# Performance work log

Hardware: AMD Instinct MI355X
Metric: run time of the kernel (lower is better)

## Reference

```python
import jax, jax.numpy as jnp
import numpy as np

B, N, DIM = 2, 2048, 1024
HEADS = 16
DIM_HEAD = DIM // HEADS  # 64
SCALE = DIM_HEAD ** -0.5


def setup_inputs() -> dict:
    key = jax.random.key(0)
    k1, k2, k3 = jax.random.split(key, 3)
    x = jax.random.normal(k1, (B, N, DIM), dtype=jnp.float32)
    W_qkv = jax.random.normal(k2, (DIM, 3 * HEADS * DIM_HEAD), dtype=jnp.float32) * (DIM ** -0.5)
    W_out = jax.random.normal(k3, (HEADS * DIM_HEAD, DIM), dtype=jnp.float32) * (DIM ** -0.5)
    return {"x": x, "W_qkv": W_qkv, "W_out": W_out}


def reference(x, W_qkv, W_out):
    b, n, _ = x.shape
    qkv = jnp.einsum('bnd,de->bne', x, W_qkv)  # [b, n, 3*h*dh]
    # faithful to einops 'b n (d k h) -> k b h n d': last axis factored as (dh, 3, h)
    qkv = qkv.reshape(b, n, DIM_HEAD, 3, HEADS)
    qkv = jnp.transpose(qkv, (3, 0, 4, 1, 2))  # [3, b, h, n, dh]
    q, k, v = qkv[0], qkv[1], qkv[2]
    scores = jnp.einsum('bhid,bhjd->bhij', q, k) * SCALE  # [b, h, n, n]
    causal_mask = jnp.triu(jnp.ones((n, n), dtype=bool), k=1)
    scores = jnp.where(causal_mask, -jnp.inf, scores)
    attn = jax.nn.softmax(scores, axis=-1)
    out = jnp.einsum('bhij,bhjd->bhid', attn, v)  # [b, h, n, dh]
    out = jnp.transpose(out, (0, 2, 1, 3)).reshape(b, n, HEADS * DIM_HEAD)  # 'b h n d -> b n (h d)'
    return jnp.einsum('bne,ed->bnd', out, W_out)
```

## Files before the change

### kernel.cpp

```cpp
#include <hip/hip_runtime.h>

typedef _Float16 f16;
typedef f16 half8 __attribute__((ext_vector_type(8)));
typedef f16 f16x4 __attribute__((ext_vector_type(4)));
typedef float f32x4 __attribute__((ext_vector_type(4)));

#define GLOAD_LDS16(gsrc, ldst)                                                              \
  __builtin_amdgcn_global_load_lds((const __attribute__((address_space(1))) void*)(gsrc),    \
                                   (__attribute__((address_space(3))) void*)(ldst), 16, 0, 0)

constexpr float SCALE = 0.125f;

__global__ __launch_bounds__(256) void k_cvt(const float4* __restrict__ in,
                                             f16x4* __restrict__ out, int n4) {
  int i = blockIdx.x * 256 + threadIdx.x;
  if (i < n4) {
    float4 v = in[i];
    f16x4 o;
    o[0] = (f16)v.x; o[1] = (f16)v.y; o[2] = (f16)v.z; o[3] = (f16)v.w;
    out[i] = o;
  }
}

__global__ __launch_bounds__(256) void k_transpose(const float* __restrict__ in,
                                                   f16* __restrict__ out, int R, int C) {
  __shared__ float t[32][33];
  int c0 = blockIdx.x * 32, r0 = blockIdx.y * 32;
  int tx = threadIdx.x, ty = threadIdx.y;
  for (int i = ty; i < 32; i += 8) t[i][tx] = in[(size_t)(r0 + i) * C + c0 + tx];
  __syncthreads();
  for (int i = ty; i < 32; i += 8) out[(size_t)(c0 + i) * R + r0 + tx] = (f16)t[tx][i];
}

template <int MODE>
__global__ __launch_bounds__(256) void k_gemm(const f16* __restrict__ A,
                                              const f16* __restrict__ Bt,
                                              float* __restrict__ C,
                                              f16* __restrict__ Qp,
                                              f16* __restrict__ Kp,
                                              f16* __restrict__ Vt) {
  constexpr int K = 1024, BK = 64;
  __shared__ alignas(16) f16 As[128 * BK];
  __shared__ alignas(16) f16 Bs[128 * BK];
  const int tid = threadIdx.x;
  const int w = tid >> 6, lane = tid & 63;
  const int g = lane >> 4, lr = lane & 15;
  const int wr = w >> 1, wc = w & 1;
  const int m0 = blockIdx.y * 128, n0 = blockIdx.x * 128;
  const int srow = lane >> 3;
  const int scol = ((lane & 7) ^ srow) << 3;

  f32x4 acc[4][4] = {};

  for (int kt = 0; kt < K; kt += BK) {
    __syncthreads();
#pragma unroll
    for (int i = 0; i < 4; ++i) {
      const int chunk = w * 4 + i;
      const int row = chunk * 8 + srow;
      GLOAD_LDS16(A + (size_t)(m0 + row) * K + kt + scol, &As[chunk * 512]);
      GLOAD_LDS16(Bt + (size_t)(n0 + row) * K + kt + scol, &Bs[chunk * 512]);
    }
    __syncthreads();
#pragma unroll
    for (int c = 0; c < 2; ++c) {
      half8 af[4], bf[4];
#pragma unroll
      for (int m = 0; m < 4; ++m) {
        const int ra = wr * 64 + m * 16 + lr;
        const int off = ra * 128 + ((((c << 2) | g) ^ (ra & 7)) << 4);
        af[m] = *(const half8*)((const char*)As + off);
      }
#pragma unroll
      for (int n = 0; n < 4; ++n) {
        const int rb = wc * 64 + n * 16 + lr;
        const int off = rb * 128 + ((((c << 2) | g) ^ (rb & 7)) << 4);
        bf[n] = *(const half8*)((const char*)Bs + off);
      }
#pragma unroll
      for (int m = 0; m < 4; ++m)
#pragma unroll
        for (int n = 0; n < 4; ++n)
          acc[m][n] = __builtin_amdgcn_mfma_f32_16x16x32_f16(af[m], bf[n], acc[m][n], 0, 0, 0);
    }
  }

  if constexpr (MODE == 0) {
#pragma unroll
    for (int m = 0; m < 4; ++m) {
      const int trow = m0 + wr * 64 + m * 16 + 4 * g;
#pragma unroll
      for (int n = 0; n < 4; ++n) {
        const int e = n0 + wc * 64 + n * 16 + lr;
        const int d = e / 48;
        const int rem = e - d * 48;
        const int wh = rem >> 4, h = rem & 15;
#pragma unroll
        for (int r = 0; r < 4; ++r) {
          const int tok = trow + r;
          const int bh = ((tok >> 11) << 4) + h;
          const int nn = tok & 2047;
          const float v = acc[m][n][r];
          if (wh == 0)
            Qp[((size_t)bh * 2048 + nn) * 64 + d] = (f16)(v * SCALE);
          else if (wh == 1)
            Kp[((size_t)bh * 2048 + nn) * 64 + d] = (f16)v;
          else
            Vt[((size_t)bh * 64 + d) * 2048 + nn] = (f16)v;
        }
      }
    }
  } else {
#pragma unroll
    for (int m = 0; m < 4; ++m)
#pragma unroll
      for (int n = 0; n < 4; ++n)
#pragma unroll
        for (int r = 0; r < 4; ++r)
          C[(size_t)(m0 + wr * 64 + m * 16 + 4 * g + r) * 1024 +
            (n0 + wc * 64 + n * 16 + lr)] = acc[m][n][r];
  }
}

__global__ __launch_bounds__(256, 2) void k_attn(const f16* __restrict__ Q,
                                                 const f16* __restrict__ Kp,
                                                 const f16* __restrict__ Vt,
                                                 f16* __restrict__ O) {
  __shared__ alignas(16) f16 plds_all[4][2][16][72];
  const int tid = threadIdx.x;
  const int w = tid >> 6, lane = tid & 63;
  const int g = lane >> 4, lr = lane & 15;
  const int bh = blockIdx.x & 31;
  const int u = blockIdx.x >> 5;
  const int t = (u < 8) ? u : 23 - u;
  const int q0 = t * 128 + w * 32;
  f16(*plds)[16][72] = plds_all[w];

  const f16* __restrict__ Qb = Q + (size_t)bh * (2048 * 64);
  const f16* __restrict__ Kb = Kp + (size_t)bh * (2048 * 64);
  const f16* __restrict__ Vb = Vt + (size_t)bh * (64 * 2048);

  half8 qf[2][2];
#pragma unroll
  for (int f = 0; f < 2; ++f)
#pragma unroll
    for (int c = 0; c < 2; ++c)
      qf[f][c] = *(const half8*)(Qb + (size_t)(q0 + 16 * f + lr) * 64 + 32 * c + 8 * g);

  f32x4 acc[2][4] = {};
  float mrow[2][4], lrow[2][4];
#pragma unroll
  for (int f = 0; f < 2; ++f)
#pragma unroll
    for (int r = 0; r < 4; ++r) {
      mrow[f][r] = -INFINITY;
      lrow[f][r] = 0.f;
    }

  const int ntiles = (q0 + 31) / 64 + 1;

  half8 kc[4][2], kn[4][2];
#pragma unroll
  for (int j = 0; j < 4; ++j)
#pragma unroll
    for (int c = 0; c < 2; ++c)
      kc[j][c] = *(const half8*)(Kb + (size_t)(16 * j + lr) * 64 + 32 * c + 8 * g);

  for (int kt = 0; kt < ntiles; ++kt) {
    const int k0 = kt * 64;
    half8 va[4][2];
#pragma unroll
    for (int nb = 0; nb < 4; ++nb)
#pragma unroll
      for (int c = 0; c < 2; ++c)
        va[nb][c] = *(const half8*)(Vb + (size_t)(16 * nb + lr) * 2048 + k0 + 32 * c + 8 * g);
    const int knext = (kt + 1 < ntiles ? kt + 1 : kt) * 64;
#pragma unroll
    for (int j = 0; j < 4; ++j)
#pragma unroll
      for (int c = 0; c < 2; ++c)
        kn[j][c] = *(const half8*)(Kb + (size_t)(knext + 16 * j + lr) * 64 + 32 * c + 8 * g);

    f32x4 s[2][4];
#pragma unroll
    for (int f = 0; f < 2; ++f)
#pragma unroll
      for (int j = 0; j < 4; ++j) {
        f32x4 z = {};
        z = __builtin_amdgcn_mfma_f32_16x16x32_f16(qf[f][0], kc[j][0], z, 0, 0, 0);
        s[f][j] = __builtin_amdgcn_mfma_f32_16x16x32_f16(qf[f][1], kc[j][1], z, 0, 0, 0);
      }

    if (k0 + 63 > q0) {
#pragma unroll
      for (int f = 0; f < 2; ++f)
#pragma unroll
        for (int j = 0; j < 4; ++j) {
          const int key = k0 + 16 * j + lr;
#pragma unroll
          for (int r = 0; r < 4; ++r)
            if (key > q0 + 16 * f + 4 * g + r) s[f][j][r] = -INFINITY;
        }
    }

#pragma unroll
    for (int f = 0; f < 2; ++f)
#pragma unroll
      for (int r = 0; r < 4; ++r) {
        float tmax = fmaxf(fmaxf(s[f][0][r], s[f][1][r]), fmaxf(s[f][2][r], s[f][3][r]));
        tmax = fmaxf(tmax, __shfl_xor(tmax, 1));
        tmax = fmaxf(tmax, __shfl_xor(tmax, 2));
        tmax = fmaxf(tmax, __shfl_xor(tmax, 4));
        tmax = fmaxf(tmax, __shfl_xor(tmax, 8));
        const float mn = fmaxf(mrow[f][r], tmax);
        const float sf = __expf(mrow[f][r] - mn);
        mrow[f][r] = mn;
        float rs = 0.f;
#pragma unroll
        for (int j = 0; j < 4; ++j) {
          const float pv = __expf(s[f][j][r] - mn);
          s[f][j][r] = pv;
          rs += pv;
        }
        rs += __shfl_xor(rs, 1);
        rs += __shfl_xor(rs, 2);
        rs += __shfl_xor(rs, 4);
        rs += __shfl_xor(rs, 8);
        lrow[f][r] = lrow[f][r] * sf + rs;
#pragma unroll
        for (int nb = 0; nb < 4; ++nb) acc[f][nb][r] *= sf;
      }

#pragma unroll
    for (int f = 0; f < 2; ++f)
#pragma unroll
      for (int j = 0; j < 4; ++j)
#pragma unroll
        for (int r = 0; r < 4; ++r)
          plds[f][4 * g + r][16 * j + lr] = (f16)s[f][j][r];
    asm volatile("s_waitcnt lgkmcnt(0)" ::: "memory");
    __builtin_amdgcn_sched_barrier(0);
    half8 pf[2][2];
#pragma unroll
    for (int f = 0; f < 2; ++f)
#pragma unroll
      for (int c = 0; c < 2; ++c)
        pf[f][c] = *(const half8*)(&plds[f][lr][32 * c + 8 * g]);

#pragma unroll
    for (int f = 0; f < 2; ++f)
#pragma unroll
      for (int nb = 0; nb < 4; ++nb) {
        acc[f][nb] = __builtin_amdgcn_mfma_f32_16x16x32_f16(pf[f][0], va[nb][0], acc[f][nb], 0, 0, 0);
        acc[f][nb] = __builtin_amdgcn_mfma_f32_16x16x32_f16(pf[f][1], va[nb][1], acc[f][nb], 0, 0, 0);
      }
    __builtin_amdgcn_sched_barrier(0);

#pragma unroll
    for (int j = 0; j < 4; ++j)
#pragma unroll
      for (int c = 0; c < 2; ++c)
        kc[j][c] = kn[j][c];
  }

  const int b = bh >> 4, h = bh & 15;
#pragma unroll
  for (int f = 0; f < 2; ++f)
#pragma unroll
    for (int r = 0; r < 4; ++r) {
      const float inv = 1.f / lrow[f][r];
      const int q = q0 + 16 * f + 4 * g + r;
      f16* orow = O + ((size_t)(b * 2048 + q) * 1024) + h * 64;
#pragma unroll
      for (int nb = 0; nb < 4; ++nb) orow[16 * nb + lr] = (f16)(acc[f][nb][r] * inv);
    }
}

extern "C" void kernel_launch(void* const* d_in, const int* in_sizes, int n_in,
                              void* d_out, int out_size, void* d_ws, size_t ws_size,
                              hipStream_t stream) {
  const float* x = (const float*)d_in[0];
  const float* Wqkv = (const float*)d_in[1];
  const float* Wout = (const float*)d_in[2];

  char* p = (char*)d_ws;
  f16* Xb = (f16*)p;    p += (size_t)4096 * 1024 * 2;
  f16* Wqkvt = (f16*)p; p += (size_t)3072 * 1024 * 2;
  f16* Woutt = (f16*)p; p += (size_t)1024 * 1024 * 2;
  f16* Qp = (f16*)p;    p += (size_t)32 * 2048 * 64 * 2;
  f16* Kp = (f16*)p;    p += (size_t)32 * 2048 * 64 * 2;
  f16* Vt = (f16*)p;    p += (size_t)32 * 64 * 2048 * 2;
  f16* O = (f16*)p;     p += (size_t)4096 * 1024 * 2;

  k_cvt<<<4096, 256, 0, stream>>>((const float4*)x, (f16x4*)Xb, 4096 * 1024 / 4);
  k_transpose<<<dim3(96, 32), dim3(32, 8), 0, stream>>>(Wqkv, Wqkvt, 1024, 3072);
  k_transpose<<<dim3(32, 32), dim3(32, 8), 0, stream>>>(Wout, Woutt, 1024, 1024);
  k_gemm<0><<<dim3(24, 32), 256, 0, stream>>>(Xb, Wqkvt, nullptr, Qp, Kp, Vt);
  k_attn<<<512, 256, 0, stream>>>(Qp, Kp, Vt, O);
  k_gemm<1><<<dim3(8, 32), 256, 0, stream>>>(O, Woutt, (float*)d_out, nullptr, nullptr, nullptr);
}
```

Before: 272.8 us.

## Permute QKV weight columns so GEMM epilogue writes contiguous Q/K/V tiles

The W_qkv transpose kernel now reorders output columns into [section][head][dim] order, so each 128-column GEMM tile belongs to a single Q, K or V section with contiguous heads. The QKV GEMM epilogue drops the per-element divide-by-48 and three-way branch. It writes Q/K with a uniform stride, and V tiles are transposed through swizzled shared memory so Vt is written with 16-byte vector stores. The goal is to replace scattered 2-byte stores with more coalesced writes, at the cost of extra barriers and LDS reuse in the V path.

```diff
diff --git a/kernel.cpp b/kernel.cpp
--- a/kernel.cpp
+++ b/kernel.cpp
@@ -32,6 +32,22 @@
   for (int i = ty; i < 32; i += 8) out[(size_t)(c0 + i) * R + r0 + tx] = (f16)t[tx][i];
 }
 
+__global__ __launch_bounds__(256) void k_transpose_qkv(const float* __restrict__ in,
+                                                       f16* __restrict__ out) {
+  __shared__ float t[32][33];
+  int c0 = blockIdx.x * 32, r0 = blockIdx.y * 32;
+  int tx = threadIdx.x, ty = threadIdx.y;
+  for (int i = ty; i < 32; i += 8) t[i][tx] = in[(size_t)(r0 + i) * 3072 + c0 + tx];
+  __syncthreads();
+  for (int i = ty; i < 32; i += 8) {
+    const int e = c0 + i;
+    const int d = e / 48, rem = e - d * 48;
+    const int k = rem >> 4, h = rem & 15;
+    const int ep = k * 1024 + h * 64 + d;
+    out[(size_t)ep * 1024 + r0 + tx] = (f16)t[tx][i];
+  }
+}
+
 template <int MODE>
 __global__ __launch_bounds__(256) void k_gemm(const f16* __restrict__ A,
                                               const f16* __restrict__ Bt,
@@ -40,8 +56,9 @@
                                               f16* __restrict__ Kp,
                                               f16* __restrict__ Vt) {
   constexpr int K = 1024, BK = 64;
-  __shared__ alignas(16) f16 As[128 * BK];
-  __shared__ alignas(16) f16 Bs[128 * BK];
+  __shared__ alignas(16) f16 smem[128 * 128];
+  f16* As = smem;
+  f16* Bs = smem + 128 * 64;
   const int tid = threadIdx.x;
   const int w = tid >> 6, lane = tid & 63;
   const int g = lane >> 4, lr = lane & 15;
@@ -86,28 +103,48 @@
   }
 
   if constexpr (MODE == 0) {
-#pragma unroll
-    for (int m = 0; m < 4; ++m) {
-      const int trow = m0 + wr * 64 + m * 16 + 4 * g;
+    const int sec = n0 >> 10;
+    const int base = n0 & 1023;
+    const int b = m0 >> 11;
+    if (sec < 2) {
+      f16* __restrict__ dst = (sec == 0) ? Qp : Kp;
+      const float mul = (sec == 0) ? SCALE : 1.0f;
 #pragma unroll
       for (int n = 0; n < 4; ++n) {
-        const int e = n0 + wc * 64 + n * 16 + lr;
-        const int d = e / 48;
-        const int rem = e - d * 48;
-        const int wh = rem >> 4, h = rem & 15;
-#pragma unroll
-        for (int r = 0; r < 4; ++r) {
-          const int tok = trow + r;
-          const int bh = ((tok >> 11) << 4) + h;
-          const int nn = tok & 2047;
-          const float v = acc[m][n][r];
-          if (wh == 0)
-            Qp[((size_t)bh * 2048 + nn) * 64 + d] = (f16)(v * SCALE);
-          else if (wh == 1)
-            Kp[((size_t)bh * 2048 + nn) * 64 + d] = (f16)v;
-          else
-            Vt[((size_t)bh * 64 + d) * 2048 + nn] = (f16)v;
+        const int idx = base + wc * 64 + n * 16 + lr;
+        const int h = idx >> 6, d = idx & 63;
+        f16* __restrict__ dh = dst + ((size_t)(b * 16 + h) * 2048) * 64 + d;
+#pragma unroll
+        for (int m = 0; m < 4; ++m)
+#pragma unroll
+          for (int r = 0; r < 4; ++r) {
+            const int nn = (m0 & 2047) + wr * 64 + m * 16 + 4 * g + r;
+            dh[(size_t)nn * 64] = (f16)(acc[m][n][r] * mul);
+          }
+      }
+    } else {
+      char* sb = (char*)smem;
+      __syncthreads();
+#pragma unroll
+      for (int m = 0; m < 4; ++m)
+#pragma unroll
+        for (int n = 0; n < 4; ++n) {
+          const int col = wc * 64 + n * 16 + lr;
+          const int tok0 = wr * 64 + m * 16 + 4 * g;
+          f16x4 v4;
+#pragma unroll
+          for (int r = 0; r < 4; ++r) v4[r] = (f16)acc[m][n][r];
+          *(f16x4*)(sb + col * 256 + ((tok0 * 2) ^ ((col & 15) << 4))) = v4;
         }
+      __syncthreads();
+      const int nn0 = m0 & 2047;
+#pragma unroll
+      for (int pass = 0; pass < 8; ++pass) {
+        const int c = w * 32 + pass * 4 + g;
+        const int idx = base + c;
+        const int h = idx >> 6, d = idx & 63;
+        const half8 v = *(const half8*)(sb + c * 256 + ((lr * 16) ^ ((c & 15) << 4)));
+        *(half8*)(Vt + ((size_t)(b * 16 + h) * 64 + d) * 2048 + nn0 + lr * 8) = v;
       }
     }
   } else {
@@ -293,7 +330,7 @@
   f16* O = (f16*)p;     p += (size_t)4096 * 1024 * 2;
 
   k_cvt<<<4096, 256, 0, stream>>>((const float4*)x, (f16x4*)Xb, 4096 * 1024 / 4);
-  k_transpose<<<dim3(96, 32), dim3(32, 8), 0, stream>>>(Wqkv, Wqkvt, 1024, 3072);
+  k_transpose_qkv<<<dim3(96, 32), dim3(32, 8), 0, stream>>>(Wqkv, Wqkvt);
   k_transpose<<<dim3(32, 32), dim3(32, 8), 0, stream>>>(Wout, Woutt, 1024, 1024);
   k_gemm<0><<<dim3(24, 32), 256, 0, stream>>>(Xb, Wqkvt, nullptr, Qp, Kp, Vt);
   k_attn<<<512, 256, 0, stream>>>(Qp, Kp, Vt, O);
```

Result: faster. 221.8 us (-18.7%).
